# Kernel optimization log

Measured on AMD Instinct MI355X. Metric: run time of the kernel, lower is better.

The kernel has to match this reference:

```python
import jax, jax.numpy as jnp
import numpy as np

NG, ND = 50000, 20000
EG, ED = 300000, 150000
FG = FD = 256
H = 256
FC = 2048
B = 65536
EPS = 1e-5


def _lrelu(x):
    return jnp.where(x >= 0, x, 0.01 * x)


def _bn(x, g, b):
    # BatchNorm1d in training mode: biased batch stats over the node dim
    m = x.mean(axis=0)
    v = ((x - m) ** 2).mean(axis=0)
    return (x - m) * jax.lax.rsqrt(v + EPS) * g + b


def _gconv(x, edge_index, Wr, br, Ws, n_nodes):
    # PyG GraphConv: out = lin_rel(sum_{j->i} x_j) + lin_root(x_i)
    src, dst = edge_index[0], edge_index[1]
    agg = jax.ops.segment_sum(x[src], dst, num_segments=n_nodes)  # [N, in]
    return agg @ Wr + br + x @ Ws


def setup_inputs() -> dict:
    key = jax.random.key(0)
    ks = iter(jax.random.split(key, 64))
    d = {}
    d["gene_x"] = jax.random.normal(next(ks), (NG, FG), jnp.float32)
    d["disease_x"] = jax.random.normal(next(ks), (ND, FD), jnp.float32)
    d["gene_edge_index"] = jax.random.randint(next(ks), (2, EG), 0, NG, jnp.int32)
    d["disease_edge_index"] = jax.random.randint(next(ks), (2, ED), 0, ND, jnp.int32)
    d["batch_idx"] = jax.random.randint(next(ks), (B, 2), 0, ND, jnp.int32)

    def lin(fin, fout):
        s = 1.0 / np.sqrt(fin)
        W = jax.random.uniform(next(ks), (fin, fout), jnp.float32, -s, s)
        b = jax.random.uniform(next(ks), (fout,), jnp.float32, -s, s)
        return W, b

    for p, fin in (("g", FG), ("d", FD)):
        for i in range(3):
            f = fin if i == 0 else H
            Wr, br = lin(f, H)
            Ws, _ = lin(f, H)
            d[f"{p}{i}_Wr"], d[f"{p}{i}_br"], d[f"{p}{i}_Ws"] = Wr, br, Ws
            d[f"bn{p}{i}_g"] = jnp.ones((H,), jnp.float32)
            d[f"bn{p}{i}_b"] = jnp.zeros((H,), jnp.float32)
    d["lin1_W"], d["lin1_b"] = lin(2 * H, FC)
    d["lin2_W"], d["lin2_b"] = lin(FC, FC // 2)
    d["lin3_W"], d["lin3_b"] = lin(FC // 2, FC // 4)
    d["lin4_W"], d["lin4_b"] = lin(FC // 4, 2)
    return d


def reference(gene_x, disease_x, gene_edge_index, disease_edge_index, batch_idx,
              g0_Wr, g0_br, g0_Ws, g1_Wr, g1_br, g1_Ws, g2_Wr, g2_br, g2_Ws,
              d0_Wr, d0_br, d0_Ws, d1_Wr, d1_br, d1_Ws, d2_Wr, d2_br, d2_Ws,
              bng0_g, bng0_b, bng1_g, bng1_b, bng2_g, bng2_b,
              bnd0_g, bnd0_b, bnd1_g, bnd1_b, bnd2_g, bnd2_b,
              lin1_W, lin1_b, lin2_W, lin2_b, lin3_W, lin3_b, lin4_W, lin4_b):
    # gene tower
    g0 = _bn(_lrelu(_gconv(gene_x, gene_edge_index, g0_Wr, g0_br, g0_Ws, NG)), bng0_g, bng0_b)
    g1 = _bn(_lrelu(_gconv(g0, gene_edge_index, g1_Wr, g1_br, g1_Ws, NG)), bng1_g, bng1_b)
    g2 = _bn(_lrelu(_gconv(g1, gene_edge_index, g2_Wr, g2_br, g2_Ws, NG)), bng2_g, bng2_b)
    gene_out = 0.7 * g0 + 0.2 * g1 + 0.1 * g2
    # disease tower
    h0 = _bn(_lrelu(_gconv(disease_x, disease_edge_index, d0_Wr, d0_br, d0_Ws, ND)), bnd0_g, bnd0_b)
    h1 = _bn(_lrelu(_gconv(h0, disease_edge_index, d1_Wr, d1_br, d1_Ws, ND)), bnd1_g, bnd1_b)
    h2 = _bn(_lrelu(_gconv(h1, disease_edge_index, d2_Wr, d2_br, d2_Ws, ND)), bnd2_g, bnd2_b)
    dis_out = 0.7 * h0 + 0.2 * h1 + 0.1 * h2
    # pair gather + MLP head (dropout is identity in eval)
    x = jnp.concatenate([gene_out[batch_idx[:, 0]], dis_out[batch_idx[:, 1]]], axis=1)
    x = _lrelu(x @ lin1_W + lin1_b)
    x = _lrelu(x @ lin2_W + lin2_b)
    x = _lrelu(x @ lin3_W + lin3_b)
    return x @ lin4_W + lin4_b
```

## Files before the change

### kernel.cpp

```cpp
#include <hip/hip_runtime.h>
#include <hip/hip_bf16.h>
#include <cstdint>
#include <cstddef>

#define N_G 50000
#define N_D 20000
#define E_G 300000
#define E_D 150000
#define BATCH 65536

typedef _Float16 f16;
typedef _Float16 f16x8 __attribute__((ext_vector_type(8)));
typedef _Float16 f16x4 __attribute__((ext_vector_type(4)));
typedef float f32x4 __attribute__((ext_vector_type(4)));

__device__ __forceinline__ float clampf(float v) {
    return fminf(fmaxf(v, -60000.f), 60000.f);
}

__device__ __forceinline__ void gl_lds16(const void* g, void* l) {
    __builtin_amdgcn_global_load_lds(
        (const __attribute__((address_space(1))) unsigned int*)g,
        (__attribute__((address_space(3))) unsigned int*)l, 16, 0, 0);
}

__global__ __launch_bounds__(256) void gemm_f16(
    const f16* __restrict__ A,
    const int* __restrict__ bidx,
    const f16* __restrict__ geneT, const f16* __restrict__ disT, int rowBase,
    const f16* __restrict__ Bt, const float* __restrict__ bias,
    f16* __restrict__ C, int M, int N, int K, int relu, int CB, int RB,
    const float* __restrict__ W4, float* __restrict__ outF,
    float* __restrict__ stats)
{
    alignas(16) __shared__ f16 sA[128 * 64];
    alignas(16) __shared__ f16 sB[128 * 64];
    const int t = threadIdx.x;
    const int w = t >> 6, l = t & 63;
    const int wm = w >> 1, wn = w & 1;
    const int q = l >> 4, lr = l & 15;

    int flat = blockIdx.x;
    int cb, rb;
    if ((RB & 7) == 0) {
        int x = flat & 7, idx = flat >> 3;
        int Sx = RB >> 3;
        cb = idx % CB;
        rb = x * Sx + idx / CB;
    } else {
        cb = flat % CB;
        rb = flat / CB;
    }
    const int mBase = rb * 128, nBase = cb * 128;

    const int subrow = l >> 3;
    const int c = l & 7;
    const char* pA[4];
    const char* pD[4];
    const char* pB[4];
    const bool fused = (bidx != nullptr);
    const bool concat = (!fused && disT != nullptr);
    const bool twoSrc = fused || concat;
#pragma unroll
    for (int j = 0; j < 4; j++) {
        int seg = j * 4 + w;
        int lrow = seg * 8 + subrow;
        int coff = ((c ^ (lrow & 7)) << 4);
        if (fused) {
            int rg = rowBase + mBase + lrow;
            int gi = bidx[2 * rg], di = bidx[2 * rg + 1];
            pA[j] = (const char*)geneT + (size_t)gi * 512 + coff;
            pD[j] = (const char*)disT + (size_t)di * 512 + coff;
        } else if (concat) {
            int arow = mBase + lrow; if (arow > M - 1) arow = M - 1;
            pA[j] = (const char*)geneT + (size_t)arow * 512 + coff;
            pD[j] = (const char*)disT + (size_t)arow * 512 + coff;
        } else {
            int arow = mBase + lrow; if (arow > M - 1) arow = M - 1;
            pA[j] = (const char*)A + (size_t)arow * K * 2 + coff;
            pD[j] = nullptr;
        }
        int brow = nBase + lrow; if (brow > N - 1) brow = N - 1;
        pB[j] = (const char*)Bt + (size_t)brow * K * 2 + coff;
    }

    f32x4 acc[4][4] = {};

    for (int k0 = 0; k0 < K; k0 += 64) {
        __syncthreads();
#pragma unroll
        for (int j = 0; j < 4; j++) {
            int seg = j * 4 + w;
            const char* srcA;
            if (twoSrc)
                srcA = (k0 < 256) ? (pA[j] + (size_t)k0 * 2) : (pD[j] + (size_t)(k0 - 256) * 2);
            else
                srcA = pA[j] + (size_t)k0 * 2;
            gl_lds16(srcA, sA + seg * 512);
            gl_lds16(pB[j] + (size_t)k0 * 2, sB + seg * 512);
        }
        __syncthreads();
        f16x8 a0[4], a1[4], b0[4], b1[4];
#pragma unroll
        for (int i = 0; i < 4; i++) {
            int r = wm * 64 + i * 16 + lr;
            int rs = r * 64;
            int x0 = (q ^ (r & 7)) << 3;
            int x1 = ((4 + q) ^ (r & 7)) << 3;
            a0[i] = *(const f16x8*)(sA + rs + x0);
            a1[i] = *(const f16x8*)(sA + rs + x1);
        }
#pragma unroll
        for (int jj = 0; jj < 4; jj++) {
            int r = wn * 64 + jj * 16 + lr;
            int rs = r * 64;
            int x0 = (q ^ (r & 7)) << 3;
            int x1 = ((4 + q) ^ (r & 7)) << 3;
            b0[jj] = *(const f16x8*)(sB + rs + x0);
            b1[jj] = *(const f16x8*)(sB + rs + x1);
        }
#pragma unroll
        for (int i = 0; i < 4; i++)
#pragma unroll
            for (int jj = 0; jj < 4; jj++) {
                acc[i][jj] = __builtin_amdgcn_mfma_f32_16x16x32_f16(a0[i], b0[jj], acc[i][jj], 0, 0, 0);
                acc[i][jj] = __builtin_amdgcn_mfma_f32_16x16x32_f16(a1[i], b1[jj], acc[i][jj], 0, 0, 0);
            }
    }

    if (W4 != nullptr) {
        float w40[4], w41[4];
#pragma unroll
        for (int j = 0; j < 4; j++) {
            int col = nBase + wn * 64 + j * 16 + lr;
            w40[j] = W4[col * 2];
            w41[j] = W4[col * 2 + 1];
        }
#pragma unroll
        for (int i = 0; i < 4; i++) {
#pragma unroll
            for (int r = 0; r < 4; r++) {
                int row = mBase + wm * 64 + i * 16 + q * 4 + r;
                float s0 = 0.f, s1 = 0.f;
#pragma unroll
                for (int j = 0; j < 4; j++) {
                    int col = nBase + wn * 64 + j * 16 + lr;
                    float v = acc[i][j][r] + bias[col];
                    v = v >= 0.f ? v : 0.01f * v;
                    v = clampf(v);
                    s0 += v * w40[j];
                    s1 += v * w41[j];
                }
#pragma unroll
                for (int off = 1; off < 16; off <<= 1) {
                    s0 += __shfl_xor(s0, off);
                    s1 += __shfl_xor(s1, off);
                }
                if (lr == 0 && row < M) {
                    atomicAdd(&outF[(size_t)(rowBase + row) * 2], s0);
                    atomicAdd(&outF[(size_t)(rowBase + row) * 2 + 1], s1);
                }
            }
        }
        return;
    }

    __syncthreads();
    f16* lt = ((w >> 1) ? sB : sA) + (w & 1) * 4096;

    float bj[4];
#pragma unroll
    for (int j = 0; j < 4; j++)
        bj[j] = bias ? bias[nBase + wn * 64 + j * 16 + lr] : 0.f;

    float sj[4] = {0.f, 0.f, 0.f, 0.f}, s2j[4] = {0.f, 0.f, 0.f, 0.f};
#pragma unroll
    for (int i = 0; i < 4; i++)
#pragma unroll
        for (int j = 0; j < 4; j++) {
            int col = j * 16 + lr;
#pragma unroll
            for (int r = 0; r < 4; r++) {
                int row = i * 16 + q * 4 + r;
                float v = acc[i][j][r] + bj[j];
                if (relu) v = v >= 0.f ? v : 0.01f * v;
                v = clampf(v);
                if (stats && (mBase + wm * 64 + row) < M) { sj[j] += v; s2j[j] += v * v; }
                int cs = col ^ ((((row >> 2) & 3) << 4) ^ ((row & 3) << 3));
                lt[row * 64 + cs] = (f16)v;
            }
        }

    if (stats) {
#pragma unroll
        for (int j = 0; j < 4; j++) {
            float s = sj[j], s2 = s2j[j];
            s += __shfl_xor(s, 16); s2 += __shfl_xor(s2, 16);
            s += __shfl_xor(s, 32); s2 += __shfl_xor(s2, 32);
            if (q == 0) {
                int col = nBase + wn * 64 + j * 16 + lr;
                if (col < 256 && col < N) {
                    atomicAdd(&stats[col], s);
                    atomicAdd(&stats[256 + col], s2);
                }
            }
        }
    }
    __syncthreads();

    const int rr = l >> 3;
    const int c8 = l & 7;
#pragma unroll
    for (int it = 0; it < 8; it++) {
        int row = it * 8 + rr;
        int cs = (c8 * 8) ^ ((((row >> 2) & 3) << 4) ^ ((row & 3) << 3));
        f16x8 vv = *(const f16x8*)(lt + row * 64 + cs);
        int grow = mBase + wm * 64 + row;
        if (grow < M)
            *(f16x8*)(C + (size_t)grow * N + nBase + wn * 64 + c8 * 8) = vv;
    }
}

__global__ __launch_bounds__(512) void gemm256(
    const f16* __restrict__ A,
    const int* __restrict__ bidx,
    const f16* __restrict__ geneT, const f16* __restrict__ disT, int rowBase,
    const f16* __restrict__ Bt, const float* __restrict__ bias,
    f16* __restrict__ C, int M, int N, int K, int relu, int CB, int RB)
{
    alignas(16) __shared__ f16 sm[65536];
    const int t = threadIdx.x;
    const int w = t >> 6, l = t & 63;
    const int wm = w >> 2, wn = w & 3;
    const int q = l >> 4, lr = l & 15;

    int flat = blockIdx.x;
    int cb, rb;
    if ((RB & 7) == 0) {
        int x = flat & 7, idx = flat >> 3;
        int Sx = RB >> 3;
        cb = idx % CB;
        rb = x * Sx + idx / CB;
    } else {
        cb = flat % CB;
        rb = flat / CB;
    }
    const int mBase = rb * 256, nBase = cb * 256;

    const int subrow = l >> 3;
    const int c = l & 7;
    const bool gat = (bidx != nullptr);
    const char* pA[4];
    const char* pD[4];
    const char* pB[4];
#pragma unroll
    for (int jj = 0; jj < 4; jj++) {
        int arow = jj * 64 + w * 8 + subrow;
        int coff = ((c ^ (arow & 7)) << 4);
        if (gat) {
            int rg = rowBase + mBase + arow;
            int gi = bidx[2 * rg], di = bidx[2 * rg + 1];
            pA[jj] = (const char*)geneT + (size_t)gi * 512 + coff;
            pD[jj] = (const char*)disT + (size_t)di * 512 + coff;
        } else {
            int ga = mBase + arow; if (ga > M - 1) ga = M - 1;
            pA[jj] = (const char*)A + (size_t)ga * K * 2 + coff;
            pD[jj] = nullptr;
        }
        int gb = nBase + arow; if (gb > N - 1) gb = N - 1;
        pB[jj] = (const char*)Bt + (size_t)gb * K * 2 + coff;
    }

    auto stage = [&](int cbuf, int k0) {
        f16* bA = sm + cbuf * 32768;
        f16* bB = bA + 16384;
#pragma unroll
        for (int jj = 0; jj < 4; jj++) {
            int R0 = jj * 64 + w * 8;
            const char* srcA;
            if (gat)
                srcA = (k0 < 256) ? (pA[jj] + (size_t)k0 * 2) : (pD[jj] + (size_t)(k0 - 256) * 2);
            else
                srcA = pA[jj] + (size_t)k0 * 2;
            gl_lds16(srcA, bA + R0 * 64);
            gl_lds16(pB[jj] + (size_t)k0 * 2, bB + R0 * 64);
        }
    };

    f32x4 acc[8][4] = {};
    const int nkt = K >> 6;

    stage(0, 0);
    int cur = 0;
    for (int kt = 0; kt < nkt; kt++) {
        if (kt + 1 < nkt) {
            stage(cur ^ 1, (kt + 1) << 6);
            asm volatile("s_waitcnt vmcnt(8)" ::: "memory");
        } else {
            asm volatile("s_waitcnt vmcnt(0)" ::: "memory");
        }
        __builtin_amdgcn_s_barrier();
        __builtin_amdgcn_sched_barrier(0);
        const f16* bA = sm + cur * 32768;
        const f16* bB = bA + 16384;
#pragma unroll
        for (int ks = 0; ks < 2; ks++) {
            f16x8 bf[4];
#pragma unroll
            for (int nf = 0; nf < 4; nf++) {
                int rB = wn * 64 + nf * 16 + lr;
                bf[nf] = *(const f16x8*)(bB + rB * 64 + ((((ks << 2) + q) ^ (rB & 7)) << 3));
            }
#pragma unroll
            for (int mf = 0; mf < 8; mf++) {
                int rA = wm * 128 + mf * 16 + lr;
                f16x8 af = *(const f16x8*)(bA + rA * 64 + ((((ks << 2) + q) ^ (rA & 7)) << 3));
#pragma unroll
                for (int nf = 0; nf < 4; nf++)
                    acc[mf][nf] = __builtin_amdgcn_mfma_f32_16x16x32_f16(af, bf[nf], acc[mf][nf], 0, 0, 0);
            }
        }
        __builtin_amdgcn_sched_barrier(0);
        __builtin_amdgcn_s_barrier();
        cur ^= 1;
    }
    __builtin_amdgcn_sched_barrier(0);

    f16* lt = sm + w * 8192;
    float bj[4];
#pragma unroll
    for (int nf = 0; nf < 4; nf++)
        bj[nf] = bias ? bias[nBase + wn * 64 + nf * 16 + lr] : 0.f;

#pragma unroll
    for (int mf = 0; mf < 8; mf++)
#pragma unroll
        for (int nf = 0; nf < 4; nf++) {
            int col = nf * 16 + lr;
#pragma unroll
            for (int r = 0; r < 4; r++) {
                int row = mf * 16 + q * 4 + r;
                float v = acc[mf][nf][r] + bj[nf];
                if (relu) v = v >= 0.f ? v : 0.01f * v;
                v = clampf(v);
                int cs = col ^ ((((row >> 2) & 3) << 4) ^ ((row & 3) << 3));
                lt[row * 64 + cs] = (f16)v;
            }
        }

    const int rr = l >> 3;
    const int c8 = l & 7;
#pragma unroll
    for (int it = 0; it < 16; it++) {
        int row = it * 8 + rr;
        int cs = (c8 * 8) ^ ((((row >> 2) & 3) << 4) ^ ((row & 3) << 3));
        f16x8 vv = *(const f16x8*)(lt + row * 64 + cs);
        int grow = mBase + wm * 128 + row;
        if (grow < M)
            *(f16x8*)(C + (size_t)grow * N + nBase + wn * 64 + c8 * 8) = vv;
    }
}

__global__ void cvt_f32_f16(const float* __restrict__ in, f16* __restrict__ out, size_t n) {
    size_t i = ((size_t)blockIdx.x * 256 + threadIdx.x) * 8;
    if (i >= n) return;
    f32x4 a = *(const f32x4*)(in + i);
    f32x4 b = *(const f32x4*)(in + i + 4);
    f16x8 o;
    o[0] = (f16)clampf(a.x); o[1] = (f16)clampf(a.y);
    o[2] = (f16)clampf(a.z); o[3] = (f16)clampf(a.w);
    o[4] = (f16)clampf(b.x); o[5] = (f16)clampf(b.y);
    o[6] = (f16)clampf(b.z); o[7] = (f16)clampf(b.w);
    *(f16x8*)(out + i) = o;
}

__global__ void init_out(const float* __restrict__ b4, float* __restrict__ out, int n) {
    int i = blockIdx.x * 256 + threadIdx.x;
    if (i < n) out[i] = b4[i & 1];
}

__global__ void count_deg(const int* __restrict__ ei, int E, int* __restrict__ deg) {
    int e = blockIdx.x * 256 + threadIdx.x;
    if (e < E) atomicAdd(&deg[ei[E + e]], 1);
}

__global__ void scan_deg(const int* __restrict__ deg, int* __restrict__ rowptr, int Nn) {
    __shared__ int part[1024];
    const int t = threadIdx.x;
    const int C = (Nn + 1023) >> 10;
    const int base = t * C;
    int s = 0;
    for (int i = 0; i < C; i++) { int idx = base + i; if (idx < Nn) s += deg[idx]; }
    part[t] = s;
    __syncthreads();
    for (int off = 1; off < 1024; off <<= 1) {
        int v = (t >= off) ? part[t - off] : 0;
        __syncthreads();
        part[t] += v;
        __syncthreads();
    }
    int pre = (t == 0) ? 0 : part[t - 1];
    for (int i = 0; i < C; i++) {
        int idx = base + i;
        if (idx < Nn) { rowptr[idx] = pre; pre += deg[idx]; }
    }
    if (t == 1023) rowptr[Nn] = part[1023];
}

__global__ void fill_csr(const int* __restrict__ ei, int E, const int* __restrict__ rowptr,
                         int* __restrict__ cursor, int* __restrict__ csr) {
    int e = blockIdx.x * 256 + threadIdx.x;
    if (e < E) {
        int d = ei[E + e];
        int p = rowptr[d] + atomicAdd(&cursor[d], 1);
        csr[p] = ei[e];
    }
}

__global__ void agg_x(const int* __restrict__ rowptr, const int* __restrict__ csr,
                      const f16* __restrict__ X, f16* __restrict__ XA, int Nn) {
    int gid = blockIdx.x * 256 + threadIdx.x;
    int node = gid >> 6, l = gid & 63;
    if (node >= Nn) return;
    int beg = rowptr[node], end = rowptr[node + 1];
    float s0 = 0.f, s1 = 0.f, s2 = 0.f, s3 = 0.f;
    for (int e = beg; e < end; e++) {
        int src = csr[e];
        f16x4 xv = *(const f16x4*)(X + (size_t)src * 256 + l * 4);
        s0 += (float)xv.x; s1 += (float)xv.y; s2 += (float)xv.z; s3 += (float)xv.w;
    }
    f16x4 o;
    o.x = (f16)clampf(s0); o.y = (f16)clampf(s1);
    o.z = (f16)clampf(s2); o.w = (f16)clampf(s3);
    *(f16x4*)(XA + (size_t)node * 256 + l * 4) = o;
}

__global__ void transpose_tile(const float* __restrict__ W, f16* __restrict__ WT,
                               int K, int N, int dstRowOff, int dstColOff, int LK) {
    __shared__ float tile[32][33];
    int n0 = blockIdx.x * 32, k0 = blockIdx.y * 32;
    int tx = threadIdx.x, ty = threadIdx.y;
    for (int yy = ty; yy < 32; yy += 8) {
        int k = k0 + yy, n = n0 + tx;
        tile[yy][tx] = (k < K && n < N) ? W[(size_t)k * N + n] : 0.f;
    }
    __syncthreads();
    for (int yy = ty; yy < 32; yy += 8) {
        int n = n0 + yy, k = k0 + tx;
        if (n < N && k < K)
            WT[(size_t)(dstRowOff + n) * LK + dstColOff + k] = (f16)clampf(tile[tx][yy]);
    }
}

__global__ void bn_apply(f16* __restrict__ y, const float* __restrict__ stats,
                         const float* __restrict__ g, const float* __restrict__ b,
                         float invN, float w, f16* __restrict__ acc, size_t total,
                         int initAcc) {
    size_t i = ((size_t)blockIdx.x * 256 + threadIdx.x) * 8;
    if (i >= total) return;
    int colb = (int)(i & 255);
    f16x8 yv = *(const f16x8*)(y + i);
    f16x8 av = {};
    if (!initAcc) av = *(const f16x8*)(acc + i);
    f16x8 yo, ao;
#pragma unroll
    for (int j = 0; j < 8; j++) {
        int col = colb + j;
        float m = stats[col] * invN;
        float var = stats[256 + col] * invN - m * m;
        if (var < 0.f) var = 0.f;
        float rs = 1.0f / sqrtf(var + 1e-5f);
        float v = ((float)yv[j] - m) * rs * g[col] + b[col];
        v = clampf(v);
        yo[j] = (f16)v;
        float p = initAcc ? 0.f : (float)av[j];
        ao[j] = (f16)clampf(p + w * v);
    }
    *(f16x8*)(y + i) = yo;
    *(f16x8*)(acc + i) = ao;
}

extern "C" void kernel_launch(void* const* d_in, const int* in_sizes, int n_in,
                              void* d_out, int out_size, void* d_ws, size_t ws_size,
                              hipStream_t stream) {
    char* ws = (char*)d_ws;
    size_t off = 0;
    auto alloc = [&](size_t bytes) -> void* {
        void* p = ws + off;
        off += (bytes + 255) & ~(size_t)255;
        return p;
    };

    f16* gene_out = (f16*)alloc((size_t)N_G * 256 * 2);
    f16* dis_out  = (f16*)alloc((size_t)N_D * 256 * 2);
    f16* W1T = (f16*)alloc((size_t)2048 * 512 * 2);
    f16* W2T = (f16*)alloc((size_t)1024 * 2048 * 2);
    f16* W3T = (f16*)alloc((size_t)512 * 1024 * 2);
    f16* WcatT = (f16*)alloc((size_t)256 * 512 * 2);
    int* csr = (int*)alloc((size_t)E_G * 4);
    int* rowptr = (int*)alloc((size_t)(N_G + 1) * 4);
    int* cnt = (int*)alloc((size_t)N_G * 4);
    float* stats = (float*)alloc(512 * 4);

    char* scratch = ws + off;
    size_t avail = (ws_size > off) ? (ws_size - off) : 0;

    f16* ybA = (f16*)scratch;
    f16* ybB = ybA + (size_t)N_G * 256;
    f16* XAbuf = ybB + (size_t)N_G * 256;

    int R = 32768;
    while ((size_t)R * 6144 > avail && R > 256) R >>= 1;
    int chunks = BATCH / R;
    f16* h1 = (f16*)scratch;
    f16* h2 = h1 + (size_t)R * 2048;

    const float* gene_x = (const float*)d_in[0];
    const float* disease_x = (const float*)d_in[1];
    const int* g_ei = (const int*)d_in[2];
    const int* d_ei = (const int*)d_in[3];
    const int* bidx = (const int*)d_in[4];
    float* out = (float*)d_out;

    const float wl[3] = {0.7f, 0.2f, 0.1f};

    auto run_tower = [&](const float* xin, const int* ei, int Nn, int E, int pbase, f16* tout) {
        size_t nelem = (size_t)Nn * 256;
        cvt_f32_f16<<<(int)((nelem / 8 + 255) / 256), 256, 0, stream>>>(xin, ybA, nelem);
        hipMemsetAsync(cnt, 0, (size_t)Nn * 4, stream);
        count_deg<<<(E + 255) / 256, 256, 0, stream>>>(ei, E, cnt);
        scan_deg<<<1, 1024, 0, stream>>>(cnt, rowptr, Nn);
        hipMemsetAsync(cnt, 0, (size_t)Nn * 4, stream);
        fill_csr<<<(E + 255) / 256, 256, 0, stream>>>(ei, E, rowptr, cnt, csr);
        f16* yin = ybA;
        f16* yout = ybB;
        int RB = (Nn + 127) / 128;
        int RBp = (RB + 7) & ~7;
        for (int l = 0; l < 3; l++) {
            const float* Wr = (const float*)d_in[pbase + l * 5 + 0];
            const float* br = (const float*)d_in[pbase + l * 5 + 1];
            const float* Wss = (const float*)d_in[pbase + l * 5 + 2];
            const float* bg = (const float*)d_in[pbase + l * 5 + 3];
            const float* bb = (const float*)d_in[pbase + l * 5 + 4];
            transpose_tile<<<dim3(8, 8), dim3(32, 8), 0, stream>>>(Wss, WcatT, 256, 256, 0, 0, 512);
            transpose_tile<<<dim3(8, 8), dim3(32, 8), 0, stream>>>(Wr, WcatT, 256, 256, 0, 256, 512);
            agg_x<<<(Nn * 64 + 255) / 256, 256, 0, stream>>>(rowptr, csr, yin, XAbuf, Nn);
            hipMemsetAsync(stats, 0, 512 * 4, stream);
            gemm_f16<<<2 * RBp, 256, 0, stream>>>(nullptr, nullptr, yin, XAbuf, 0,
                                                  WcatT, br, yout, Nn, 256, 512, 1, 2, RBp,
                                                  nullptr, nullptr, stats);
            bn_apply<<<(int)((nelem / 8 + 255) / 256), 256, 0, stream>>>(
                yout, stats, bg, bb, 1.0f / Nn, wl[l], tout, nelem, l == 0);
            f16* tmp = yin; yin = yout; yout = tmp;
        }
    };

    run_tower(gene_x, g_ei, N_G, E_G, 5, gene_out);
    run_tower(disease_x, d_ei, N_D, E_D, 20, dis_out);

    const float* lin1_W = (const float*)d_in[35];
    const float* lin1_b = (const float*)d_in[36];
    const float* lin2_W = (const float*)d_in[37];
    const float* lin2_b = (const float*)d_in[38];
    const float* lin3_W = (const float*)d_in[39];
    const float* lin3_b = (const float*)d_in[40];
    const float* lin4_W = (const float*)d_in[41];
    const float* lin4_b = (const float*)d_in[42];

    transpose_tile<<<dim3(64, 16), dim3(32, 8), 0, stream>>>(lin1_W, W1T, 512, 2048, 0, 0, 512);
    transpose_tile<<<dim3(32, 64), dim3(32, 8), 0, stream>>>(lin2_W, W2T, 2048, 1024, 0, 0, 2048);
    transpose_tile<<<dim3(16, 32), dim3(32, 8), 0, stream>>>(lin3_W, W3T, 1024, 512, 0, 0, 1024);
    init_out<<<(BATCH * 2 + 255) / 256, 256, 0, stream>>>(lin4_b, out, BATCH * 2);

    for (int c = 0; c < chunks; c++) {
        int rb = c * R;
        if ((R & 255) == 0) {
            int RB2 = R / 256;
            gemm256<<<8 * RB2, 512, 0, stream>>>(nullptr, bidx, gene_out, dis_out, rb,
                                                 W1T, lin1_b, h1, R, 2048, 512, 1, 8, RB2);
            gemm256<<<4 * RB2, 512, 0, stream>>>(h1, nullptr, nullptr, nullptr, 0,
                                                 W2T, lin2_b, h2, R, 1024, 2048, 1, 4, RB2);
        } else {
            int RB = R / 128;
            gemm_f16<<<16 * RB, 256, 0, stream>>>(nullptr, bidx, gene_out, dis_out, rb,
                                                  W1T, lin1_b, h1, R, 2048, 512, 1, 16, RB,
                                                  nullptr, nullptr, nullptr);
            gemm_f16<<<8 * RB, 256, 0, stream>>>(h1, nullptr, nullptr, nullptr, 0,
                                                 W2T, lin2_b, h2, R, 1024, 2048, 1, 8, RB,
                                                 nullptr, nullptr, nullptr);
        }
        int RB = R / 128;
        gemm_f16<<<4 * RB, 256, 0, stream>>>(h2, nullptr, nullptr, nullptr, rb,
                                             W3T, lin3_b, nullptr, R, 512, 1024, 1, 4, RB,
                                             lin4_W, out, nullptr);
    }
}
```

Before: 1.484 ms.

## Triple-buffer A tiles with two-stage prefetch in gemm256

Splits the staging of A and B tiles and gives A three LDS buffers, so A (which may be a random gather of gene/disease rows) is prefetched two k-steps ahead while B stays double-buffered. The wait counts are adjusted so only the current tile's loads must complete. This hides more of the latency of the irregular gathered loads, at the cost of 160KB of LDS per block (up from 128KB), which still allows only one block per CU.

```diff
diff --git a/kernel.cpp b/kernel.cpp
--- a/kernel.cpp
+++ b/kernel.cpp
@@ -228,7 +228,7 @@
     const f16* __restrict__ Bt, const float* __restrict__ bias,
     f16* __restrict__ C, int M, int N, int K, int relu, int CB, int RB)
 {
-    alignas(16) __shared__ f16 sm[65536];
+    alignas(16) __shared__ f16 sm[81920];
     const int t = threadIdx.x;
     const int w = t >> 6, l = t & 63;
     const int wm = w >> 2, wn = w & 3;
@@ -271,9 +271,11 @@
         pB[jj] = (const char*)Bt + (size_t)gb * K * 2 + coff;
     }
 
-    auto stage = [&](int cbuf, int k0) {
-        f16* bA = sm + cbuf * 32768;
-        f16* bB = bA + 16384;
+    f16* const smA = sm;
+    f16* const smB = sm + 3 * 16384;
+
+    auto stageA = [&](int abuf, int k0) {
+        f16* bA = smA + abuf * 16384;
 #pragma unroll
         for (int jj = 0; jj < 4; jj++) {
             int R0 = jj * 64 + w * 8;
@@ -283,6 +285,13 @@
             else
                 srcA = pA[jj] + (size_t)k0 * 2;
             gl_lds16(srcA, bA + R0 * 64);
+        }
+    };
+    auto stageB = [&](int bbuf, int k0) {
+        f16* bB = smB + bbuf * 16384;
+#pragma unroll
+        for (int jj = 0; jj < 4; jj++) {
+            int R0 = jj * 64 + w * 8;
             gl_lds16(pB[jj] + (size_t)k0 * 2, bB + R0 * 64);
         }
     };
@@ -290,19 +299,20 @@
     f32x4 acc[8][4] = {};
     const int nkt = K >> 6;
 
-    stage(0, 0);
-    int cur = 0;
+    stageA(0, 0);
+    stageB(0, 0);
+    if (nkt > 1) stageA(1, 64);
+
     for (int kt = 0; kt < nkt; kt++) {
-        if (kt + 1 < nkt) {
-            stage(cur ^ 1, (kt + 1) << 6);
-            asm volatile("s_waitcnt vmcnt(8)" ::: "memory");
-        } else {
-            asm volatile("s_waitcnt vmcnt(0)" ::: "memory");
-        }
+        if (kt + 1 < nkt) stageB((kt + 1) & 1, (kt + 1) << 6);
+        if (kt + 2 < nkt) stageA((kt + 2) % 3, (kt + 2) << 6);
+        if (kt + 2 < nkt)      asm volatile("s_waitcnt vmcnt(12)" ::: "memory");
+        else if (kt + 1 < nkt) asm volatile("s_waitcnt vmcnt(8)" ::: "memory");
+        else                   asm volatile("s_waitcnt vmcnt(0)" ::: "memory");
         __builtin_amdgcn_s_barrier();
         __builtin_amdgcn_sched_barrier(0);
-        const f16* bA = sm + cur * 32768;
-        const f16* bB = bA + 16384;
+        const f16* bA = smA + (kt % 3) * 16384;
+        const f16* bB = smB + (kt & 1) * 16384;
 #pragma unroll
         for (int ks = 0; ks < 2; ks++) {
             f16x8 bf[4];
@@ -322,7 +332,6 @@
         }
         __builtin_amdgcn_sched_barrier(0);
         __builtin_amdgcn_s_barrier();
-        cur ^= 1;
     }
     __builtin_amdgcn_sched_barrier(0);
 
```

New measurement: 1.467 ms. About the same (-1.2%).

## Single-buffer gemm256 LDS and split epilogue into halves to halve shared memory

Applied to the files above, without the earlier changes.

Removes double buffering of the A/B tiles in the 256x256 GEMM, cutting LDS from 128KB to 64KB. Each k-step now loads synchronously between two __syncthreads. The epilogue writes the accumulator tile in two halves to fit the smaller staging area. The aim is to fit two workgroups per CU and gain occupancy, but global loads no longer overlap with MFMA work inside a block.

```diff
diff --git a/kernel.cpp b/kernel.cpp
--- a/kernel.cpp
+++ b/kernel.cpp
@@ -228,7 +228,7 @@
     const f16* __restrict__ Bt, const float* __restrict__ bias,
     f16* __restrict__ C, int M, int N, int K, int relu, int CB, int RB)
 {
-    alignas(16) __shared__ f16 sm[65536];
+    alignas(16) __shared__ f16 sm[32768];
     const int t = threadIdx.x;
     const int w = t >> 6, l = t & 63;
     const int wm = w >> 2, wn = w & 3;
@@ -271,9 +271,15 @@
         pB[jj] = (const char*)Bt + (size_t)gb * K * 2 + coff;
     }
 
-    auto stage = [&](int cbuf, int k0) {
-        f16* bA = sm + cbuf * 32768;
-        f16* bB = bA + 16384;
+    f16* const sA = sm;
+    f16* const sB = sm + 16384;
+
+    f32x4 acc[8][4] = {};
+    const int nkt = K >> 6;
+
+    for (int kt = 0; kt < nkt; kt++) {
+        const int k0 = kt << 6;
+        __syncthreads();
 #pragma unroll
         for (int jj = 0; jj < 4; jj++) {
             int R0 = jj * 64 + w * 8;
@@ -282,82 +288,67 @@
                 srcA = (k0 < 256) ? (pA[jj] + (size_t)k0 * 2) : (pD[jj] + (size_t)(k0 - 256) * 2);
             else
                 srcA = pA[jj] + (size_t)k0 * 2;
-            gl_lds16(srcA, bA + R0 * 64);
-            gl_lds16(pB[jj] + (size_t)k0 * 2, bB + R0 * 64);
-        }
-    };
-
-    f32x4 acc[8][4] = {};
-    const int nkt = K >> 6;
-
-    stage(0, 0);
-    int cur = 0;
-    for (int kt = 0; kt < nkt; kt++) {
-        if (kt + 1 < nkt) {
-            stage(cur ^ 1, (kt + 1) << 6);
-            asm volatile("s_waitcnt vmcnt(8)" ::: "memory");
-        } else {
-            asm volatile("s_waitcnt vmcnt(0)" ::: "memory");
-        }
-        __builtin_amdgcn_s_barrier();
-        __builtin_amdgcn_sched_barrier(0);
-        const f16* bA = sm + cur * 32768;
-        const f16* bB = bA + 16384;
+            gl_lds16(srcA, sA + R0 * 64);
+            gl_lds16(pB[jj] + (size_t)k0 * 2, sB + R0 * 64);
+        }
+        __syncthreads();
 #pragma unroll
         for (int ks = 0; ks < 2; ks++) {
             f16x8 bf[4];
 #pragma unroll
             for (int nf = 0; nf < 4; nf++) {
                 int rB = wn * 64 + nf * 16 + lr;
-                bf[nf] = *(const f16x8*)(bB + rB * 64 + ((((ks << 2) + q) ^ (rB & 7)) << 3));
+                bf[nf] = *(const f16x8*)(sB + rB * 64 + ((((ks << 2) + q) ^ (rB & 7)) << 3));
             }
 #pragma unroll
             for (int mf = 0; mf < 8; mf++) {
                 int rA = wm * 128 + mf * 16 + lr;
-                f16x8 af = *(const f16x8*)(bA + rA * 64 + ((((ks << 2) + q) ^ (rA & 7)) << 3));
+                f16x8 af = *(const f16x8*)(sA + rA * 64 + ((((ks << 2) + q) ^ (rA & 7)) << 3));
 #pragma unroll
                 for (int nf = 0; nf < 4; nf++)
                     acc[mf][nf] = __builtin_amdgcn_mfma_f32_16x16x32_f16(af, bf[nf], acc[mf][nf], 0, 0, 0);
             }
         }
-        __builtin_amdgcn_sched_barrier(0);
-        __builtin_amdgcn_s_barrier();
-        cur ^= 1;
-    }
-    __builtin_amdgcn_sched_barrier(0);
-
-    f16* lt = sm + w * 8192;
+    }
+
+    f16* lt = sm + w * 4096;
     float bj[4];
 #pragma unroll
     for (int nf = 0; nf < 4; nf++)
         bj[nf] = bias ? bias[nBase + wn * 64 + nf * 16 + lr] : 0.f;
 
-#pragma unroll
-    for (int mf = 0; mf < 8; mf++)
-#pragma unroll
-        for (int nf = 0; nf < 4; nf++) {
-            int col = nf * 16 + lr;
-#pragma unroll
-            for (int r = 0; r < 4; r++) {
-                int row = mf * 16 + q * 4 + r;
-                float v = acc[mf][nf][r] + bj[nf];
-                if (relu) v = v >= 0.f ? v : 0.01f * v;
-                v = clampf(v);
-                int cs = col ^ ((((row >> 2) & 3) << 4) ^ ((row & 3) << 3));
-                lt[row * 64 + cs] = (f16)v;
-            }
-        }
-
     const int rr = l >> 3;
     const int c8 = l & 7;
 #pragma unroll
-    for (int it = 0; it < 16; it++) {
-        int row = it * 8 + rr;
-        int cs = (c8 * 8) ^ ((((row >> 2) & 3) << 4) ^ ((row & 3) << 3));
-        f16x8 vv = *(const f16x8*)(lt + row * 64 + cs);
-        int grow = mBase + wm * 128 + row;
-        if (grow < M)
-            *(f16x8*)(C + (size_t)grow * N + nBase + wn * 64 + c8 * 8) = vv;
+    for (int half = 0; half < 2; half++) {
+        __syncthreads();
+#pragma unroll
+        for (int mh = 0; mh < 4; mh++) {
+            int mf = half * 4 + mh;
+#pragma unroll
+            for (int nf = 0; nf < 4; nf++) {
+                int col = nf * 16 + lr;
+#pragma unroll
+                for (int r = 0; r < 4; r++) {
+                    int row = mh * 16 + q * 4 + r;
+                    float v = acc[mf][nf][r] + bj[nf];
+                    if (relu) v = v >= 0.f ? v : 0.01f * v;
+                    v = clampf(v);
+                    int cs = col ^ ((((row >> 2) & 3) << 4) ^ ((row & 3) << 3));
+                    lt[row * 64 + cs] = (f16)v;
+                }
+            }
+        }
+        __syncthreads();
+#pragma unroll
+        for (int it = 0; it < 8; it++) {
+            int row = it * 8 + rr;
+            int cs = (c8 * 8) ^ ((((row >> 2) & 3) << 4) ^ ((row & 3) << 3));
+            f16x8 vv = *(const f16x8*)(lt + row * 64 + cs);
+            int grow = mBase + wm * 128 + half * 64 + row;
+            if (grow < M)
+                *(f16x8*)(C + (size_t)grow * N + nBase + wn * 64 + c8 * 8) = vv;
+        }
     }
 }
 
```

Result: slower. 1.538 ms (+3.6%).
